# Performance work log

Hardware: AMD Instinct MI355X
Metric: run time of the kernel (lower is better)

Reference implementation:

```python
import jax, jax.numpy as jnp
import numpy as np

N, NS, D, HID = 8192, 512, 1024, 1024  # nodes, num_edges, f_dim, mlp hidden (max(f_dim,128))


def layernorm(x, g, b, eps=1e-5):
    m = x.mean(-1, keepdims=True)
    v = x.var(-1, keepdims=True)
    return (x - m) / jnp.sqrt(v + eps) * g + b


def mask_topk(a, kk):
    # keep only the top-kk entries of each row (vectorized version of mask_attn)
    _, idx = jax.lax.top_k(a, kk)
    rows = jnp.arange(a.shape[0])[:, None]
    mask = jnp.zeros(a.shape, a.dtype).at[rows, idx].set(1.0)
    return a * mask


def setup_inputs() -> dict:
    key = jax.random.key(0)
    ks = jax.random.split(key, 16)
    xavier = lambda k, i, o: jax.random.uniform(k, (i, o), jnp.float32, -1.0, 1.0) * np.sqrt(6.0 / (i + o))
    return {
        "inputs": jax.random.normal(ks[0], (N, D), jnp.float32),
        "noise": jax.random.normal(ks[1], (NS, D), jnp.float32),
        "edges_mu": jax.random.normal(ks[2], (1, D), jnp.float32),
        "edges_logsigma": xavier(ks[3], 1, D),
        "Wq": xavier(ks[4], D, D), "bq": jnp.zeros((D,), jnp.float32),
        "Wk": xavier(ks[5], D, D), "bk": jnp.zeros((D,), jnp.float32),
        "Wv": xavier(ks[6], D, D), "bv": jnp.zeros((D,), jnp.float32),
        "W1": xavier(ks[7], 2 * D, HID), "b1": jnp.zeros((HID,), jnp.float32),
        "W2": xavier(ks[8], HID, D), "b2": jnp.zeros((D,), jnp.float32),
        "g_in": jnp.ones((D,), jnp.float32), "b_in": jnp.zeros((D,), jnp.float32),
        "g_e": jnp.ones((D,), jnp.float32), "b_e": jnp.zeros((D,), jnp.float32),
        "k_n": 64,
        "k_e": 8,
    }


def reference(inputs, noise, edges_mu, edges_logsigma, Wq, bq, Wk, bk, Wv, bv,
              W1, b1, W2, b2, g_in, b_in, g_e, b_e, k_n, k_e):
    n, d = inputs.shape
    scale = d ** -0.5
    eps = 1e-8
    x = layernorm(inputs, g_in, b_in)                       # norm_input
    k = jax.nn.relu(x @ Wk + bk)                            # [N, D]
    v = jax.nn.relu(x @ Wv + bv)                            # [N, D]
    edges = edges_mu + jnp.exp(edges_logsigma) * noise      # [NS, D]
    # single iteration (iters=1)
    edges = layernorm(edges, g_e, b_e)                      # norm_edgs
    q = jax.nn.relu(edges @ Wq + bq)                        # [NS, D]
    dots = jnp.einsum('ni,mi->nm', q, k) * scale            # [NS, N]
    attn = jax.nn.softmax(dots, axis=1) + eps
    attn = attn / attn.sum(axis=1, keepdims=True)
    attn = mask_topk(attn, k_n)
    updates = jnp.einsum('nm,md->nd', attn, v)              # [NS, D]
    edges = jnp.concatenate([edges, updates], axis=1)       # [NS, 2D]
    edges = jax.nn.relu(edges @ W1 + b1) @ W2 + b2          # mlp -> [NS, D]
    q2 = x @ Wq + bq                                        # no relu in source
    k2 = jax.nn.relu(edges @ Wk + bk)                       # [NS, D]
    dots_v = jnp.einsum('ni,mi->nm', q2, k2) * scale        # [N, NS]
    attn_v = jax.nn.softmax(dots_v, axis=1)
    H = mask_topk(attn_v, k_e)
    return edges, H, dots
```

## Files before the change

### kernel.cpp

```cpp
#include <hip/hip_runtime.h>
#include <stdint.h>
#include <stddef.h>

typedef unsigned short u16;
typedef __bf16 bf16x8 __attribute__((ext_vector_type(8)));
typedef float f32x4 __attribute__((ext_vector_type(4)));

#define DEV __device__ __forceinline__

DEV float bf2f(u16 u){ union{uint32_t i; float f;} c; c.i=(uint32_t)u<<16; return c.f; }
DEV u16 f2bf(float f){ union{float f; uint32_t i;} c; c.f=f; uint32_t x=c.i;
  uint32_t r = x + 0x7FFFu + ((x>>16)&1u); return (u16)(r>>16); }
DEV uint32_t fmap(float f){ union{float f; uint32_t u;} c; c.f=f;
  return (c.u & 0x80000000u) ? ~c.u : (c.u | 0x80000000u); }
DEV float funmap(uint32_t u){ union{uint32_t u; float f;} c;
  c.u = (u & 0x80000000u) ? (u & 0x7FFFFFFFu) : ~u; return c.f; }
DEV void split2(float x, u16& h, u16& l){ h = f2bf(x); l = f2bf(x - bf2f(h)); }

DEV float bredsum(float v, float* buf, int tid){
  #pragma unroll
  for(int o=32;o;o>>=1) v += __shfl_down(v,o);
  __syncthreads();
  if((tid&63)==0) buf[tid>>6]=v;
  __syncthreads();
  return buf[0]+buf[1]+buf[2]+buf[3];
}
DEV float bredmax(float v, float* buf, int tid){
  #pragma unroll
  for(int o=32;o;o>>=1) v = fmaxf(v, __shfl_down(v,o));
  __syncthreads();
  if((tid&63)==0) buf[tid>>6]=v;
  __syncthreads();
  return fmaxf(fmaxf(buf[0],buf[1]),fmaxf(buf[2],buf[3]));
}
DEV int bredsumi(int v, int* buf, int tid){
  #pragma unroll
  for(int o=32;o;o>>=1) v += __shfl_down(v,o);
  __syncthreads();
  if((tid&63)==0) buf[tid>>6]=v;
  __syncthreads();
  return buf[0]+buf[1]+buf[2]+buf[3];
}

template<bool RELU, int SK>
__global__ __launch_bounds__(256)
void gemm1_64(const u16* __restrict__ A, int lda,
              const u16* __restrict__ Bt, int ldb,
              const float* __restrict__ bias, float scale,
              u16* __restrict__ outb, float* __restrict__ outf,
              float* __restrict__ part,
              int K, int ldc, int M)
{
  __shared__ __align__(16) u16 As[64*32];
  __shared__ __align__(16) u16 Bs[128*32];
  const int tid = threadIdx.x, lane = tid&63, wave = tid>>6;
  const int m0 = blockIdx.y*64, n0 = blockIdx.x*128;
  const int wm = (wave>>1)*32, wn = (wave&1)*64;
  const int ml = lane&15, quad = lane>>4;
  const int ks = K / SK;
  const int kbeg = blockIdx.z * ks;
  const u16* pa  = A  + (size_t)(m0+(tid>>2))*lda + kbeg + (tid&3)*8;
  const u16* pb0 = Bt + (size_t)(n0+(tid>>2))*ldb + kbeg + (tid&3)*8;
  const u16* pb1 = Bt + (size_t)(n0+64+(tid>>2))*ldb + kbeg + (tid&3)*8;

  f32x4 acc[2][4];
  #pragma unroll
  for(int i=0;i<2;i++)
    #pragma unroll
    for(int j=0;j<4;j++) acc[i][j] = (f32x4){0.f,0.f,0.f,0.f};

  uint4 ra=*(const uint4*)pa, rb0=*(const uint4*)pb0, rb1=*(const uint4*)pb1;
  for(int k0=0;k0<ks;k0+=32){
    __syncthreads();
    *(uint4*)&As[tid*8]       = ra;
    *(uint4*)&Bs[tid*8]       = rb0;
    *(uint4*)&Bs[(256+tid)*8] = rb1;
    __syncthreads();
    if(k0+32<ks){
      ra  = *(const uint4*)(pa +k0+32);
      rb0 = *(const uint4*)(pb0+k0+32);
      rb1 = *(const uint4*)(pb1+k0+32);
    }
    bf16x8 af[2], bf[4];
    #pragma unroll
    for(int mi=0;mi<2;mi++) af[mi] = *(const bf16x8*)&As[(wm+mi*16+ml)*32 + quad*8];
    #pragma unroll
    for(int ni=0;ni<4;ni++) bf[ni] = *(const bf16x8*)&Bs[(wn+ni*16+ml)*32 + quad*8];
    #pragma unroll
    for(int mi=0;mi<2;mi++)
      #pragma unroll
      for(int ni=0;ni<4;ni++)
        acc[mi][ni] = __builtin_amdgcn_mfma_f32_16x16x32_bf16(af[mi], bf[ni], acc[mi][ni], 0,0,0);
  }
  #pragma unroll
  for(int mi=0;mi<2;mi++){
    const int rbase = m0 + wm + mi*16 + quad*4;
    #pragma unroll
    for(int ni=0;ni<4;ni++){
      const int col = n0 + wn + ni*16 + ml;
      if(SK==1){
        const float bv = bias ? bias[col] : 0.f;
        #pragma unroll
        for(int r=0;r<4;r++){
          float v = acc[mi][ni][r]*scale + bv;
          if(RELU) v = fmaxf(v, 0.f);
          const size_t idx = (size_t)(rbase + r)*ldc + col;
          if(outb) outb[idx] = f2bf(v);
          if(outf) outf[idx] = v;
        }
      }else{
        #pragma unroll
        for(int r=0;r<4;r++)
          part[((size_t)blockIdx.z*M + rbase + r)*ldc + col] = acc[mi][ni][r];
      }
    }
  }
}

template<bool RELU>
__global__ __launch_bounds__(256)
void gemm1_128(const u16* __restrict__ A, int lda,
               const u16* __restrict__ Bt, int ldb,
               const float* __restrict__ bias, float scale,
               u16* __restrict__ outb, float* __restrict__ outf,
               int K, int ldc)
{
  __shared__ __align__(16) u16 As[128*32];
  __shared__ __align__(16) u16 Bs[128*32];
  const int tid = threadIdx.x, lane = tid&63, wave = tid>>6;
  const int m0 = blockIdx.y*128, n0 = blockIdx.x*128;
  const int wm = (wave>>1)*64, wn = (wave&1)*64;
  const int ml = lane&15, quad = lane>>4;
  const u16* pa0 = A  + (size_t)(m0+(tid>>2))*lda    + (tid&3)*8;
  const u16* pa1 = A  + (size_t)(m0+64+(tid>>2))*lda + (tid&3)*8;
  const u16* pb0 = Bt + (size_t)(n0+(tid>>2))*ldb    + (tid&3)*8;
  const u16* pb1 = Bt + (size_t)(n0+64+(tid>>2))*ldb + (tid&3)*8;

  f32x4 acc[4][4];
  #pragma unroll
  for(int i=0;i<4;i++)
    #pragma unroll
    for(int j=0;j<4;j++) acc[i][j] = (f32x4){0.f,0.f,0.f,0.f};

  uint4 ra0=*(const uint4*)pa0, ra1=*(const uint4*)pa1;
  uint4 rb0=*(const uint4*)pb0, rb1=*(const uint4*)pb1;
  for(int k0=0;k0<K;k0+=32){
    __syncthreads();
    *(uint4*)&As[tid*8]       = ra0;
    *(uint4*)&As[(256+tid)*8] = ra1;
    *(uint4*)&Bs[tid*8]       = rb0;
    *(uint4*)&Bs[(256+tid)*8] = rb1;
    __syncthreads();
    if(k0+32<K){
      ra0 = *(const uint4*)(pa0+k0+32);
      ra1 = *(const uint4*)(pa1+k0+32);
      rb0 = *(const uint4*)(pb0+k0+32);
      rb1 = *(const uint4*)(pb1+k0+32);
    }
    bf16x8 af[4], bf[4];
    #pragma unroll
    for(int mi=0;mi<4;mi++) af[mi] = *(const bf16x8*)&As[(wm+mi*16+ml)*32 + quad*8];
    #pragma unroll
    for(int ni=0;ni<4;ni++) bf[ni] = *(const bf16x8*)&Bs[(wn+ni*16+ml)*32 + quad*8];
    #pragma unroll
    for(int mi=0;mi<4;mi++)
      #pragma unroll
      for(int ni=0;ni<4;ni++)
        acc[mi][ni] = __builtin_amdgcn_mfma_f32_16x16x32_bf16(af[mi], bf[ni], acc[mi][ni], 0,0,0);
  }
  #pragma unroll
  for(int mi=0;mi<4;mi++){
    const int rbase = m0 + wm + mi*16 + quad*4;
    #pragma unroll
    for(int ni=0;ni<4;ni++){
      const int col = n0 + wn + ni*16 + ml;
      const float bv = bias ? bias[col] : 0.f;
      #pragma unroll
      for(int r=0;r<4;r++){
        float v = acc[mi][ni][r]*scale + bv;
        if(RELU) v = fmaxf(v, 0.f);
        const size_t idx = (size_t)(rbase + r)*ldc + col;
        if(outb) outb[idx] = f2bf(v);
        if(outf) outf[idx] = v;
      }
    }
  }
}

template<bool RELU, int SK>
__global__ __launch_bounds__(256)
void gemm3_64(const u16* __restrict__ Ah, const u16* __restrict__ Al, int lda,
              const u16* __restrict__ Bh, const u16* __restrict__ Bl, int ldb,
              const float* __restrict__ bias, float scale,
              u16* __restrict__ outh, u16* __restrict__ outl,
              float* __restrict__ outf, float* __restrict__ part,
              int K, int ldc, int M)
{
  __shared__ __align__(16) u16 AsH[64*32];
  __shared__ __align__(16) u16 AsL[64*32];
  __shared__ __align__(16) u16 BsH[128*32];
  __shared__ __align__(16) u16 BsL[128*32];
  const int tid = threadIdx.x, lane = tid&63, wave = tid>>6;
  const int m0 = blockIdx.y*64, n0 = blockIdx.x*128;
  const int wm = (wave>>1)*32, wn = (wave&1)*64;
  const int ml = lane&15, quad = lane>>4;
  const int ks = K / SK;
  const int kbeg = blockIdx.z * ks;
  const size_t ao  = (size_t)(m0+(tid>>2))*lda + kbeg + (tid&3)*8;
  const size_t bo0 = (size_t)(n0+(tid>>2))*ldb + kbeg + (tid&3)*8;
  const size_t bo1 = (size_t)(n0+64+(tid>>2))*ldb + kbeg + (tid&3)*8;

  f32x4 acc[2][4];
  #pragma unroll
  for(int i=0;i<2;i++)
    #pragma unroll
    for(int j=0;j<4;j++) acc[i][j] = (f32x4){0.f,0.f,0.f,0.f};

  uint4 rah=*(const uint4*)(Ah+ao),  ral=*(const uint4*)(Al+ao);
  uint4 rbh0=*(const uint4*)(Bh+bo0), rbl0=*(const uint4*)(Bl+bo0);
  uint4 rbh1=*(const uint4*)(Bh+bo1), rbl1=*(const uint4*)(Bl+bo1);
  for(int k0=0;k0<ks;k0+=32){
    __syncthreads();
    *(uint4*)&AsH[tid*8]       = rah;
    *(uint4*)&AsL[tid*8]       = ral;
    *(uint4*)&BsH[tid*8]       = rbh0;
    *(uint4*)&BsL[tid*8]       = rbl0;
    *(uint4*)&BsH[(256+tid)*8] = rbh1;
    *(uint4*)&BsL[(256+tid)*8] = rbl1;
    __syncthreads();
    if(k0+32<ks){
      const int s = k0+32;
      rah =*(const uint4*)(Ah+ao +s); ral =*(const uint4*)(Al+ao +s);
      rbh0=*(const uint4*)(Bh+bo0+s); rbl0=*(const uint4*)(Bl+bo0+s);
      rbh1=*(const uint4*)(Bh+bo1+s); rbl1=*(const uint4*)(Bl+bo1+s);
    }
    bf16x8 afh[2], afl[2], bfh[4], bfl[4];
    #pragma unroll
    for(int mi=0;mi<2;mi++){
      const int o = (wm+mi*16+ml)*32 + quad*8;
      afh[mi] = *(const bf16x8*)&AsH[o];
      afl[mi] = *(const bf16x8*)&AsL[o];
    }
    #pragma unroll
    for(int ni=0;ni<4;ni++){
      const int o = (wn+ni*16+ml)*32 + quad*8;
      bfh[ni] = *(const bf16x8*)&BsH[o];
      bfl[ni] = *(const bf16x8*)&BsL[o];
    }
    #pragma unroll
    for(int mi=0;mi<2;mi++)
      #pragma unroll
      for(int ni=0;ni<4;ni++){
        acc[mi][ni] = __builtin_amdgcn_mfma_f32_16x16x32_bf16(afh[mi], bfh[ni], acc[mi][ni], 0,0,0);
        acc[mi][ni] = __builtin_amdgcn_mfma_f32_16x16x32_bf16(afh[mi], bfl[ni], acc[mi][ni], 0,0,0);
        acc[mi][ni] = __builtin_amdgcn_mfma_f32_16x16x32_bf16(afl[mi], bfh[ni], acc[mi][ni], 0,0,0);
      }
  }
  #pragma unroll
  for(int mi=0;mi<2;mi++){
    const int rbase = m0 + wm + mi*16 + quad*4;
    #pragma unroll
    for(int ni=0;ni<4;ni++){
      const int col = n0 + wn + ni*16 + ml;
      if(SK==1){
        const float bv = bias ? bias[col] : 0.f;
        #pragma unroll
        for(int r=0;r<4;r++){
          float v = acc[mi][ni][r]*scale + bv;
          if(RELU) v = fmaxf(v, 0.f);
          const size_t idx = (size_t)(rbase + r)*ldc + col;
          if(outh){ u16 h, l; split2(v, h, l); outh[idx] = h; outl[idx] = l; }
          if(outf) outf[idx] = v;
        }
      }else{
        #pragma unroll
        for(int r=0;r<4;r++)
          part[((size_t)blockIdx.z*M + rbase + r)*ldc + col] = acc[mi][ni][r];
      }
    }
  }
}

__global__ __launch_bounds__(256)
void gemm3_128(const u16* __restrict__ Ah, const u16* __restrict__ Al, int lda,
               const u16* __restrict__ Bh, const u16* __restrict__ Bl, int ldb,
               const float* __restrict__ bias, float scale,
               float* __restrict__ outf, int K, int ldc)
{
  __shared__ __align__(16) u16 AsH[128*32];
  __shared__ __align__(16) u16 AsL[128*32];
  __shared__ __align__(16) u16 BsH[128*32];
  __shared__ __align__(16) u16 BsL[128*32];
  const int tid = threadIdx.x, lane = tid&63, wave = tid>>6;
  const int m0 = blockIdx.y*128, n0 = blockIdx.x*128;
  const int wm = (wave>>1)*64, wn = (wave&1)*64;
  const int ml = lane&15, quad = lane>>4;
  const size_t ao0 = (size_t)(m0+(tid>>2))*lda    + (tid&3)*8;
  const size_t ao1 = (size_t)(m0+64+(tid>>2))*lda + (tid&3)*8;
  const size_t bo0 = (size_t)(n0+(tid>>2))*ldb    + (tid&3)*8;
  const size_t bo1 = (size_t)(n0+64+(tid>>2))*ldb + (tid&3)*8;

  f32x4 acc[4][4];
  #pragma unroll
  for(int i=0;i<4;i++)
    #pragma unroll
    for(int j=0;j<4;j++) acc[i][j] = (f32x4){0.f,0.f,0.f,0.f};

  uint4 rah0=*(const uint4*)(Ah+ao0), ral0=*(const uint4*)(Al+ao0);
  uint4 rah1=*(const uint4*)(Ah+ao1), ral1=*(const uint4*)(Al+ao1);
  uint4 rbh0=*(const uint4*)(Bh+bo0), rbl0=*(const uint4*)(Bl+bo0);
  uint4 rbh1=*(const uint4*)(Bh+bo1), rbl1=*(const uint4*)(Bl+bo1);
  for(int k0=0;k0<K;k0+=32){
    __syncthreads();
    *(uint4*)&AsH[tid*8]       = rah0;
    *(uint4*)&AsH[(256+tid)*8] = rah1;
    *(uint4*)&AsL[tid*8]       = ral0;
    *(uint4*)&AsL[(256+tid)*8] = ral1;
    *(uint4*)&BsH[tid*8]       = rbh0;
    *(uint4*)&BsH[(256+tid)*8] = rbh1;
    *(uint4*)&BsL[tid*8]       = rbl0;
    *(uint4*)&BsL[(256+tid)*8] = rbl1;
    __syncthreads();
    if(k0+32<K){
      const int s = k0+32;
      rah0=*(const uint4*)(Ah+ao0+s); ral0=*(const uint4*)(Al+ao0+s);
      rah1=*(const uint4*)(Ah+ao1+s); ral1=*(const uint4*)(Al+ao1+s);
      rbh0=*(const uint4*)(Bh+bo0+s); rbl0=*(const uint4*)(Bl+bo0+s);
      rbh1=*(const uint4*)(Bh+bo1+s); rbl1=*(const uint4*)(Bl+bo1+s);
    }
    bf16x8 afh[4], afl[4], bfh[4], bfl[4];
    #pragma unroll
    for(int mi=0;mi<4;mi++){
      const int o = (wm+mi*16+ml)*32 + quad*8;
      afh[mi] = *(const bf16x8*)&AsH[o];
      afl[mi] = *(const bf16x8*)&AsL[o];
    }
    #pragma unroll
    for(int ni=0;ni<4;ni++){
      const int o = (wn+ni*16+ml)*32 + quad*8;
      bfh[ni] = *(const bf16x8*)&BsH[o];
      bfl[ni] = *(const bf16x8*)&BsL[o];
    }
    #pragma unroll
    for(int mi=0;mi<4;mi++)
      #pragma unroll
      for(int ni=0;ni<4;ni++){
        acc[mi][ni] = __builtin_amdgcn_mfma_f32_16x16x32_bf16(afh[mi], bfh[ni], acc[mi][ni], 0,0,0);
        acc[mi][ni] = __builtin_amdgcn_mfma_f32_16x16x32_bf16(afh[mi], bfl[ni], acc[mi][ni], 0,0,0);
        acc[mi][ni] = __builtin_amdgcn_mfma_f32_16x16x32_bf16(afl[mi], bfh[ni], acc[mi][ni], 0,0,0);
      }
  }
  #pragma unroll
  for(int mi=0;mi<4;mi++){
    const int rbase = m0 + wm + mi*16 + quad*4;
    #pragma unroll
    for(int ni=0;ni<4;ni++){
      const int col = n0 + wn + ni*16 + ml;
      const float bv = bias ? bias[col] : 0.f;
      #pragma unroll
      for(int r=0;r<4;r++){
        const float v = acc[mi][ni][r]*scale + bv;
        outf[(size_t)(rbase + r)*ldc + col] = v;
      }
    }
  }
}

template<bool RELU, int SK>
__global__ __launch_bounds__(256)
void reduce_epi(const float* __restrict__ part, const float* __restrict__ bias,
                float scale, u16* __restrict__ outh, u16* __restrict__ outl,
                u16* __restrict__ outb, float* __restrict__ outf,
                size_t MN, int N)
{
  const size_t i = ((size_t)blockIdx.x*256 + threadIdx.x)*4;
  float4 s = *(const float4*)(part + i);
  #pragma unroll
  for(int z=1; z<SK; z++){
    const float4 t = *(const float4*)(part + (size_t)z*MN + i);
    s.x += t.x; s.y += t.y; s.z += t.z; s.w += t.w;
  }
  const int col = (int)(i % (size_t)N);
  float4 bv = bias ? *(const float4*)(bias + col) : (float4){0.f,0.f,0.f,0.f};
  float v[4] = { s.x*scale + bv.x, s.y*scale + bv.y, s.z*scale + bv.z, s.w*scale + bv.w };
  if(RELU){
    #pragma unroll
    for(int j=0;j<4;j++) v[j] = fmaxf(v[j], 0.f);
  }
  if(outh){
    ushort4 h4, l4;
    split2(v[0], h4.x, l4.x); split2(v[1], h4.y, l4.y);
    split2(v[2], h4.z, l4.z); split2(v[3], h4.w, l4.w);
    *(ushort4*)(outh + i) = h4;
    *(ushort4*)(outl + i) = l4;
  }
  if(outb){
    ushort4 b4;
    b4.x=f2bf(v[0]); b4.y=f2bf(v[1]); b4.z=f2bf(v[2]); b4.w=f2bf(v[3]);
    *(ushort4*)(outb + i) = b4;
  }
  if(outf) *(float4*)(outf + i) = (float4){v[0],v[1],v[2],v[3]};
}

__global__ __launch_bounds__(256)
void transpose_split(const float* __restrict__ in, u16* __restrict__ outh,
                     u16* __restrict__ outl, int R, int C)
{
  __shared__ float tile[32][33];
  const int tx = threadIdx.x & 31, ty = threadIdx.x >> 5;
  const int bx = blockIdx.x*32, by = blockIdx.y*32;
  #pragma unroll
  for(int i=0;i<32;i+=8)
    tile[ty+i][tx] = in[(size_t)(by+ty+i)*C + bx + tx];
  __syncthreads();
  #pragma unroll
  for(int i=0;i<32;i+=8){
    const float v = tile[tx][ty+i];
    u16 h, l; split2(v, h, l);
    const size_t o = (size_t)(bx+ty+i)*R + by + tx;
    outh[o] = h; outl[o] = l;
  }
}
__global__ __launch_bounds__(256)
void transpose_plain(const float* __restrict__ in, u16* __restrict__ outh, int R, int C)
{
  __shared__ float tile[32][33];
  const int tx = threadIdx.x & 31, ty = threadIdx.x >> 5;
  const int bx = blockIdx.x*32, by = blockIdx.y*32;
  #pragma unroll
  for(int i=0;i<32;i+=8)
    tile[ty+i][tx] = in[(size_t)(by+ty+i)*C + bx + tx];
  __syncthreads();
  #pragma unroll
  for(int i=0;i<32;i+=8)
    outh[(size_t)(bx+ty+i)*R + by + tx] = f2bf(tile[tx][ty+i]);
}
__global__ __launch_bounds__(256)
void split_convert(const float* __restrict__ in, u16* __restrict__ oh,
                   u16* __restrict__ ol)
{
  const int i = blockIdx.x*256 + threadIdx.x;
  const float4 v = ((const float4*)in)[i];
  ushort4 h4, l4;
  split2(v.x, h4.x, l4.x); split2(v.y, h4.y, l4.y);
  split2(v.z, h4.z, l4.z); split2(v.w, h4.w, l4.w);
  ((ushort4*)oh)[i] = h4; ((ushort4*)ol)[i] = l4;
}

__global__ __launch_bounds__(256)
void layernorm_rows(const float* __restrict__ in, const float* __restrict__ g,
                    const float* __restrict__ bb, u16* __restrict__ outh,
                    u16* __restrict__ outl, int ostride)
{
  __shared__ float buf[4];
  const int row = blockIdx.x, tid = threadIdx.x;
  const float4 xv = ((const float4*)(in + (size_t)row*1024))[tid];
  float s  = bredsum(xv.x+xv.y+xv.z+xv.w, buf, tid);
  float s2 = bredsum(xv.x*xv.x+xv.y*xv.y+xv.z*xv.z+xv.w*xv.w, buf, tid);
  const float mean = s * (1.f/1024.f);
  const float var  = s2 * (1.f/1024.f) - mean*mean;
  const float rs   = 1.f / sqrtf(var + 1e-5f);
  const float4 gv = ((const float4*)g)[tid];
  const float4 bv = ((const float4*)bb)[tid];
  float o0 = (xv.x-mean)*rs*gv.x + bv.x;
  float o1 = (xv.y-mean)*rs*gv.y + bv.y;
  float o2 = (xv.z-mean)*rs*gv.z + bv.z;
  float o3 = (xv.w-mean)*rs*gv.w + bv.w;
  ushort4 oh, ol;
  split2(o0, oh.x, ol.x); split2(o1, oh.y, ol.y);
  split2(o2, oh.z, ol.z); split2(o3, oh.w, ol.w);
  ((ushort4*)(outh + (size_t)row*ostride))[tid] = oh;
  ((ushort4*)(outl + (size_t)row*ostride))[tid] = ol;
}

__global__ __launch_bounds__(256)
void edges_ln(const float* __restrict__ noise, const float* __restrict__ mu,
              const float* __restrict__ lsig, const float* __restrict__ g,
              const float* __restrict__ bb, u16* __restrict__ outh,
              u16* __restrict__ outl, int ostride)
{
  __shared__ float buf[4];
  const int row = blockIdx.x, tid = threadIdx.x;
  const float4 nv  = ((const float4*)(noise + (size_t)row*1024))[tid];
  const float4 muv = ((const float4*)mu)[tid];
  const float4 lsv = ((const float4*)lsig)[tid];
  float v0 = muv.x + expf(lsv.x)*nv.x;
  float v1 = muv.y + expf(lsv.y)*nv.y;
  float v2 = muv.z + expf(lsv.z)*nv.z;
  float v3 = muv.w + expf(lsv.w)*nv.w;
  float s  = bredsum(v0+v1+v2+v3, buf, tid);
  float s2 = bredsum(v0*v0+v1*v1+v2*v2+v3*v3, buf, tid);
  const float mean = s * (1.f/1024.f);
  const float var  = s2 * (1.f/1024.f) - mean*mean;
  const float rs   = 1.f / sqrtf(var + 1e-5f);
  const float4 gv = ((const float4*)g)[tid];
  const float4 bv = ((const float4*)bb)[tid];
  float o0 = (v0-mean)*rs*gv.x + bv.x;
  float o1 = (v1-mean)*rs*gv.y + bv.y;
  float o2 = (v2-mean)*rs*gv.z + bv.z;
  float o3 = (v3-mean)*rs*gv.w + bv.w;
  ushort4 oh, ol;
  split2(o0, oh.x, ol.x); split2(o1, oh.y, ol.y);
  split2(o2, oh.z, ol.z); split2(o3, oh.w, ol.w);
  ((ushort4*)(outh + (size_t)row*ostride))[tid] = oh;
  ((ushort4*)(outl + (size_t)row*ostride))[tid] = ol;
}

#define SWZ(i) ((i) ^ (((((unsigned)(i))>>5)&7u)<<2))
__global__ __launch_bounds__(256)
void softmax_topk_a(const float* __restrict__ dots, const int* __restrict__ knp,
                    int* __restrict__ tidx, float* __restrict__ tw)
{
  const int NC = 8192;
  __shared__ __align__(16) uint32_t us[8192];
  __shared__ float fbuf[4];
  __shared__ int ibuf[4];
  __shared__ int scan[256];
  __shared__ uint32_t hist[256];
  __shared__ uint32_t bcast;
  __shared__ int slot_ctr;
  const int row = blockIdx.x, tid = threadIdx.x;
  const int lane = tid & 63, wave = tid >> 6;
  const float* x = dots + (size_t)row * NC;

  float mx = -3.4e38f;
  #pragma unroll
  for(int it=0; it<8; ++it){
    const int i = (tid + it*256)*4;
    const float4 f = *(const float4*)(x + i);
    mx = fmaxf(fmaxf(mx, fmaxf(f.x,f.y)), fmaxf(f.z,f.w));
    uint4 u; u.x=fmap(f.x); u.y=fmap(f.y); u.z=fmap(f.z); u.w=fmap(f.w);
    *(uint4*)&us[SWZ(i)] = u;
  }
  mx = bredmax(mx, fbuf, tid);

  float se = 0.f;
  #pragma unroll
  for(int it=0; it<8; ++it){
    const int i = (tid + it*256)*4;
    const uint4 u = *(const uint4*)&us[SWZ(i)];
    se += expf(funmap(u.x)-mx) + expf(funmap(u.y)-mx)
        + expf(funmap(u.z)-mx) + expf(funmap(u.w)-mx);
  }
  se = bredsum(se, fbuf, tid);
  const float T = 1.f + (float)NC * 1e-8f;

  const int k = knp[0];
  const int base = tid*32;

  uint32_t prefix = 0;
  int remaining = k;
  #pragma unroll
  for(int shift=24; shift>=0; shift-=8){
    hist[tid] = 0;
    __syncthreads();
    const uint32_t himask = (shift==24) ? 0u : (0xFFFFFFFFu << (shift+8));
    #pragma unroll
    for(int j=0;j<32;j+=4){
      const uint4 u4 = *(const uint4*)&us[SWZ(base+j)];
      const uint32_t uu[4] = {u4.x,u4.y,u4.z,u4.w};
      #pragma unroll
      for(int t=0;t<4;t++)
        if((uu[t] & himask) == prefix) atomicAdd(&hist[(uu[t]>>shift)&255u], 1u);
    }
    __syncthreads();
    if(wave==0){
      const uint32_t h0=hist[4*lane], h1=hist[4*lane+1],
                     h2=hist[4*lane+2], h3=hist[4*lane+3];
      const uint32_t s3=h3, s2=h2+s3, s1=h1+s2, s0=h0+s1;
      uint32_t tsum = s0;
      #pragma unroll
      for(int o=1;o<64;o<<=1){
        const uint32_t vv = __shfl_down(tsum, o);
        if(lane + o < 64) tsum += vv;
      }
      const uint32_t excl = tsum - s0;
      const uint32_t r = (uint32_t)remaining;
      int cand = -1; uint32_t gsel = 0;
      if     (s3+excl >= r){ cand = 4*lane+3; gsel = excl; }
      else if(s2+excl >= r){ cand = 4*lane+2; gsel = s3+excl; }
      else if(s1+excl >= r){ cand = 4*lane+1; gsel = s2+excl; }
      else if(s0+excl >= r){ cand = 4*lane+0; gsel = s1+excl; }
      int bestc = cand; uint32_t bestg = gsel;
      #pragma unroll
      for(int o=32;o;o>>=1){
        const int oc = __shfl_xor(bestc, o);
        const uint32_t og = __shfl_xor(bestg, o);
        if(oc > bestc){ bestc = oc; bestg = og; }
      }
      if(lane==0) bcast = (uint32_t)bestc;
      remaining -= (int)bestg;
    }
    __syncthreads();
    prefix |= bcast << shift;
  }
  const uint32_t uth = prefix;

  int gt = 0, eq = 0;
  #pragma unroll
  for(int j=0;j<32;j+=4){
    const uint4 u4 = *(const uint4*)&us[SWZ(base+j)];
    gt += (u4.x>uth)+(u4.y>uth)+(u4.z>uth)+(u4.w>uth);
    eq += (u4.x==uth)+(u4.y==uth)+(u4.z==uth)+(u4.w==uth);
  }
  const int c1 = bredsumi(gt, ibuf, tid);
  __syncthreads();
  scan[tid] = eq;
  __syncthreads();
  #pragma unroll
  for(int o=1;o<256;o<<=1){
    int t = (tid>=o) ? scan[tid-o] : 0;
    __syncthreads();
    scan[tid] += t;
    __syncthreads();
  }
  int eq_rank = scan[tid] - eq;
  const int budget = k - c1;
  if(tid==0) slot_ctr = 0;
  __syncthreads();
  #pragma unroll 2
  for(int j=0;j<32;j+=4){
    const uint4 u4 = *(const uint4*)&us[SWZ(base+j)];
    const uint32_t uu[4] = {u4.x,u4.y,u4.z,u4.w};
    #pragma unroll
    for(int t=0;t<4;t++){
      const uint32_t u = uu[t];
      bool sel = (u > uth);
      if(u == uth){ sel = (eq_rank < budget); eq_rank++; }
      if(sel){
        const int s = atomicAdd(&slot_ctr, 1);
        const float f = funmap(u);
        const float w = (expf(f - mx)/se + 1e-8f) / T;
        if(s < 128){ tidx[row*128 + s] = base + j + t; tw[row*128 + s] = w; }
      }
    }
  }
}

__global__ __launch_bounds__(256)
void gather_updates(const int* __restrict__ tidx, const float* __restrict__ tw,
                    const int* __restrict__ knp, const u16* __restrict__ v,
                    u16* __restrict__ cath, u16* __restrict__ catl)
{
  __shared__ int   idx_s[128];
  __shared__ float w_s[128];
  const int row = blockIdx.x, tid = threadIdx.x;
  const int kk = knp[0];
  if(tid < 128){
    idx_s[tid] = (tid < kk) ? (tidx[row*128+tid] & 8191) : 0;
    w_s[tid]   = (tid < kk) ? tw[row*128+tid] : 0.f;
  }
  __syncthreads();
  const int c = tid*4;
  float a0=0,a1=0,a2=0,a3=0;
  for(int j=0;j<kk && j<128;j++){
    const ushort4 vv = *(const ushort4*)&v[(size_t)idx_s[j]*1024 + c];
    const float w = w_s[j];
    a0 += w*bf2f(vv.x); a1 += w*bf2f(vv.y); a2 += w*bf2f(vv.z); a3 += w*bf2f(vv.w);
  }
  ushort4 oh, ol;
  split2(a0, oh.x, ol.x); split2(a1, oh.y, ol.y);
  split2(a2, oh.z, ol.z); split2(a3, oh.w, ol.w);
  ((ushort4*)(cath + (size_t)row*2048 + 1024))[tid] = oh;
  ((ushort4*)(catl + (size_t)row*2048 + 1024))[tid] = ol;
}

__global__ __launch_bounds__(256)
void bias_v_kernel(const float* __restrict__ bq, const u16* __restrict__ k2h,
                   const u16* __restrict__ k2l, float* __restrict__ out)
{
  __shared__ float buf[4];
  const int row = blockIdx.x, tid = threadIdx.x;
  const ushort4 h4 = ((const ushort4*)(k2h + (size_t)row*1024))[tid];
  const ushort4 l4 = ((const ushort4*)(k2l + (size_t)row*1024))[tid];
  const float4 b4 = ((const float4*)bq)[tid];
  float s = b4.x*(bf2f(h4.x)+bf2f(l4.x)) + b4.y*(bf2f(h4.y)+bf2f(l4.y))
          + b4.z*(bf2f(h4.z)+bf2f(l4.z)) + b4.w*(bf2f(h4.w)+bf2f(l4.w));
  s = bredsum(s, buf, tid);
  if(tid==0) out[row] = s * 0.03125f;
}

__global__ __launch_bounds__(256)
void softmax_topk_h_wave(const float* __restrict__ dv, const int* __restrict__ kep,
                         float* __restrict__ H)
{
  const int wave = threadIdx.x >> 6, lane = threadIdx.x & 63;
  const int row = blockIdx.x*4 + wave;
  const float* x = dv + (size_t)row*512 + lane*8;
  const float4 a = *(const float4*)x;
  const float4 b = *(const float4*)(x+4);
  float vals[8] = {a.x,a.y,a.z,a.w,b.x,b.y,b.z,b.w};

  float mx = vals[0];
  #pragma unroll
  for(int j=1;j<8;j++) mx = fmaxf(mx, vals[j]);
  #pragma unroll
  for(int o=32;o;o>>=1) mx = fmaxf(mx, __shfl_xor(mx, o));
  float e[8], se = 0.f;
  #pragma unroll
  for(int j=0;j<8;j++){ e[j] = expf(vals[j]-mx); se += e[j]; }
  #pragma unroll
  for(int o=32;o;o>>=1) se += __shfl_xor(se, o);
  const float inv = 1.f/se;

  const int k = kep[0];
  unsigned int selmask = 0;
  for(int r=0;r<k;r++){
    unsigned long long best = 0;
    #pragma unroll
    for(int j=0;j<8;j++){
      if(!((selmask>>j)&1u)){
        const unsigned long long key =
          ((unsigned long long)fmap(vals[j]) << 9) | (unsigned long long)(511 - (lane*8+j));
        if(key > best) best = key;
      }
    }
    #pragma unroll
    for(int o=32;o;o>>=1){
      const unsigned long long other = __shfl_xor(best, o);
      if(other > best) best = other;
    }
    const int bidx = 511 - (int)(best & 511ull);
    if((bidx>>3) == lane) selmask |= 1u << (bidx & 7);
  }

  float4 o0, o1;
  o0.x = (selmask&  1u) ? e[0]*inv : 0.f;
  o0.y = (selmask&  2u) ? e[1]*inv : 0.f;
  o0.z = (selmask&  4u) ? e[2]*inv : 0.f;
  o0.w = (selmask&  8u) ? e[3]*inv : 0.f;
  o1.x = (selmask& 16u) ? e[4]*inv : 0.f;
  o1.y = (selmask& 32u) ? e[5]*inv : 0.f;
  o1.z = (selmask& 64u) ? e[6]*inv : 0.f;
  o1.w = (selmask&128u) ? e[7]*inv : 0.f;
  float* outp = H + (size_t)row*512 + lane*8;
  *(float4*)outp     = o0;
  *(float4*)(outp+4) = o1;
}

extern "C" void kernel_launch(void* const* d_in, const int* in_sizes, int n_in,
                              void* d_out, int out_size, void* d_ws, size_t ws_size,
                              hipStream_t stream)
{
  const float* inputs = (const float*)d_in[0];
  const float* noise  = (const float*)d_in[1];
  const float* emu    = (const float*)d_in[2];
  const float* elsig  = (const float*)d_in[3];
  const float* Wq = (const float*)d_in[4];  const float* bq = (const float*)d_in[5];
  const float* Wk = (const float*)d_in[6];  const float* bk = (const float*)d_in[7];
  const float* Wv = (const float*)d_in[8];  const float* bv = (const float*)d_in[9];
  const float* W1 = (const float*)d_in[10]; const float* b1 = (const float*)d_in[11];
  const float* W2 = (const float*)d_in[12]; const float* b2 = (const float*)d_in[13];
  const float* g_in = (const float*)d_in[14]; const float* b_in = (const float*)d_in[15];
  const float* g_e  = (const float*)d_in[16]; const float* b_e  = (const float*)d_in[17];
  const int* knp = (const int*)d_in[18];
  const int* kep = (const int*)d_in[19];

  float* out = (float*)d_out;
  float* out_edges = out;
  float* out_H     = out + 512*1024;
  float* out_dots  = out + 512*1024 + 8192*512;

  char* p = (char*)d_ws;
  const size_t MB = 1024ull*1024;
  u16* xh = (u16*)(p + 0*MB);
  u16* xl = (u16*)(p + 16*MB);
  u16* kb = (u16*)(p + 32*MB);
  u16* vb = (u16*)(p + 48*MB);
  float* dotsvf = (float*)(p + 32*MB);
  u16* WkTh = (u16*)(p + 64*MB);  u16* WkTl = (u16*)(p + 66*MB);
  u16* WvTh = (u16*)(p + 68*MB);
  u16* WqTh = (u16*)(p + 70*MB);
  u16* Wqh  = (u16*)(p + 72*MB);  u16* Wql  = (u16*)(p + 74*MB);
  u16* W1Th = (u16*)(p + 76*MB);  u16* W1Tl = (u16*)(p + 80*MB);
  u16* W2Th = (u16*)(p + 84*MB);  u16* W2Tl = (u16*)(p + 86*MB);
  u16* cath = (u16*)(p + 88*MB);  u16* catl = (u16*)(p + 90*MB);
  u16* qmb  = (u16*)(p + 92*MB);
  u16* h1h  = (u16*)(p + 93*MB);  u16* h1l  = (u16*)(p + 94*MB);
  u16* eoh  = (u16*)(p + 95*MB);  u16* eol  = (u16*)(p + 96*MB);
  u16* k2h  = (u16*)(p + 97*MB);  u16* k2l  = (u16*)(p + 98*MB);
  u16* Gth  = (u16*)(p + 99*MB);  u16* Gtl  = (u16*)(p + 100*MB);
  int*   tidx  = (int*)  (p + 101*MB);
  float* tw    = (float*)(p + 101*MB + 256*1024);
  float* biasv = (float*)(p + 101*MB + 512*1024);
  float* part  = (float*)(p + 104*MB);

  hipMemsetAsync(tidx, 0, 512ull*128*4, stream);
  hipMemsetAsync(tw,   0, 512ull*128*4, stream);

  transpose_split<<<dim3(32,32),256,0,stream>>>(Wk, WkTh, WkTl, 1024, 1024);
  transpose_split<<<dim3(32,64),256,0,stream>>>(W1, W1Th, W1Tl, 2048, 1024);
  transpose_split<<<dim3(32,32),256,0,stream>>>(W2, W2Th, W2Tl, 1024, 1024);
  transpose_plain<<<dim3(32,32),256,0,stream>>>(Wv, WvTh, 1024, 1024);
  transpose_plain<<<dim3(32,32),256,0,stream>>>(Wq, WqTh, 1024, 1024);
  split_convert<<<1024,256,0,stream>>>(Wq, Wqh, Wql);

  layernorm_rows<<<8192,256,0,stream>>>(inputs, g_in, b_in, xh, xl, 1024);
  edges_ln<<<512,256,0,stream>>>(noise, emu, elsig, g_e, b_e, cath, catl, 2048);

  const size_t MN = 512ull*1024;
  gemm1_128<true><<<dim3(8,64),256,0,stream>>>(xh,1024, WkTh,1024, bk, 1.f,
                                               kb,nullptr, 1024,1024);
  gemm1_128<true><<<dim3(8,64),256,0,stream>>>(xh,1024, WvTh,1024, bv, 1.f,
                                               vb,nullptr, 1024,1024);
  gemm1_64<false,4><<<dim3(8,8,4),256,0,stream>>>(cath,2048, WqTh,1024, nullptr, 1.f,
                                                  nullptr,nullptr, part, 1024,1024,512);
  reduce_epi<true,4><<<512,256,0,stream>>>(part, bq, 1.f, nullptr,nullptr, qmb,nullptr, MN, 1024);
  gemm1_128<false><<<dim3(64,4),256,0,stream>>>(qmb,1024, kb,1024, nullptr, 0.03125f,
                                                nullptr,out_dots, 1024,8192);
  softmax_topk_a<<<512,256,0,stream>>>(out_dots, knp, tidx, tw);
  gather_updates<<<512,256,0,stream>>>(tidx, tw, knp, vb, cath, catl);

  gemm3_64<false,4><<<dim3(8,8,4),256,0,stream>>>(cath,catl,2048, W1Th,W1Tl,2048,
                                                  nullptr,1.f, nullptr,nullptr,nullptr,
                                                  part, 2048,1024,512);
  reduce_epi<true,4><<<512,256,0,stream>>>(part, b1, 1.f, h1h,h1l, nullptr,nullptr, MN, 1024);
  gemm3_64<false,4><<<dim3(8,8,4),256,0,stream>>>(h1h,h1l,1024, W2Th,W2Tl,1024,
                                                  nullptr,1.f, nullptr,nullptr,nullptr,
                                                  part, 1024,1024,512);
  reduce_epi<false,4><<<512,256,0,stream>>>(part, b2, 1.f, eoh,eol, nullptr,out_edges, MN, 1024);
  gemm3_64<false,4><<<dim3(8,8,4),256,0,stream>>>(eoh,eol,1024, WkTh,WkTl,1024,
                                                  nullptr,1.f, nullptr,nullptr,nullptr,
                                                  part, 1024,1024,512);
  reduce_epi<true,4><<<512,256,0,stream>>>(part, bk, 1.f, k2h,k2l, nullptr,nullptr, MN, 1024);
  gemm3_64<false,4><<<dim3(8,8,4),256,0,stream>>>(k2h,k2l,1024, Wqh,Wql,1024,
                                                  nullptr,1.f, nullptr,nullptr,nullptr,
                                                  part, 1024,1024,512);
  reduce_epi<false,4><<<512,256,0,stream>>>(part, nullptr, 1.f, Gth,Gtl, nullptr,nullptr, MN, 1024);
  bias_v_kernel<<<512,256,0,stream>>>(bq, k2h, k2l, biasv);
  gemm3_128<<<dim3(4,64),256,0,stream>>>(xh,xl,1024, Gth,Gtl,1024,
                                         biasv, 0.03125f, dotsvf, 1024,512);
  softmax_topk_h_wave<<<2048,256,0,stream>>>(dotsvf, kep, out_H);
}
```

Measured before the change: 413.4 us.

## Fuse prep, layernorm, K/V GEMMs and bias-v into fewer kernel launches

```diff
diff --git a/kernel.cpp b/kernel.cpp
--- a/kernel.cpp
+++ b/kernel.cpp
@@ -187,6 +187,74 @@
   }
 }
 
+__global__ __launch_bounds__(256)
+void gemm_kv_128(const u16* __restrict__ A, int lda,
+                 const u16* __restrict__ Bt, int ldb,
+                 const float* __restrict__ bk, const float* __restrict__ bv,
+                 u16* __restrict__ kb, u16* __restrict__ vb, int K)
+{
+  __shared__ __align__(16) u16 As[128*32];
+  __shared__ __align__(16) u16 Bs[128*32];
+  const int tid = threadIdx.x, lane = tid&63, wave = tid>>6;
+  const int m0 = blockIdx.y*128, n0 = blockIdx.x*128;
+  const int wm = (wave>>1)*64, wn = (wave&1)*64;
+  const int ml = lane&15, quad = lane>>4;
+  const u16* pa0 = A  + (size_t)(m0+(tid>>2))*lda    + (tid&3)*8;
+  const u16* pa1 = A  + (size_t)(m0+64+(tid>>2))*lda + (tid&3)*8;
+  const u16* pb0 = Bt + (size_t)(n0+(tid>>2))*ldb    + (tid&3)*8;
+  const u16* pb1 = Bt + (size_t)(n0+64+(tid>>2))*ldb + (tid&3)*8;
+
+  f32x4 acc[4][4];
+  #pragma unroll
+  for(int i=0;i<4;i++)
+    #pragma unroll
+    for(int j=0;j<4;j++) acc[i][j] = (f32x4){0.f,0.f,0.f,0.f};
+
+  uint4 ra0=*(const uint4*)pa0, ra1=*(const uint4*)pa1;
+  uint4 rb0=*(const uint4*)pb0, rb1=*(const uint4*)pb1;
+  for(int k0=0;k0<K;k0+=32){
+    __syncthreads();
+    *(uint4*)&As[tid*8]       = ra0;
+    *(uint4*)&As[(256+tid)*8] = ra1;
+    *(uint4*)&Bs[tid*8]       = rb0;
+    *(uint4*)&Bs[(256+tid)*8] = rb1;
+    __syncthreads();
+    if(k0+32<K){
+      ra0 = *(const uint4*)(pa0+k0+32);
+      ra1 = *(const uint4*)(pa1+k0+32);
+      rb0 = *(const uint4*)(pb0+k0+32);
+      rb1 = *(const uint4*)(pb1+k0+32);
+    }
+    bf16x8 af[4], bf[4];
+    #pragma unroll
+    for(int mi=0;mi<4;mi++) af[mi] = *(const bf16x8*)&As[(wm+mi*16+ml)*32 + quad*8];
+    #pragma unroll
+    for(int ni=0;ni<4;ni++) bf[ni] = *(const bf16x8*)&Bs[(wn+ni*16+ml)*32 + quad*8];
+    #pragma unroll
+    for(int mi=0;mi<4;mi++)
+      #pragma unroll
+      for(int ni=0;ni<4;ni++)
+        acc[mi][ni] = __builtin_amdgcn_mfma_f32_16x16x32_bf16(af[mi], bf[ni], acc[mi][ni], 0,0,0);
+  }
+  #pragma unroll
+  for(int mi=0;mi<4;mi++){
+    const int rbase = m0 + wm + mi*16 + quad*4;
+    #pragma unroll
+    for(int ni=0;ni<4;ni++){
+      const int col = n0 + wn + ni*16 + ml;
+      const bool isv = col >= 1024;
+      const int c2 = col & 1023;
+      const float bb = isv ? bv[c2] : bk[c2];
+      u16* outp = isv ? vb : kb;
+      #pragma unroll
+      for(int r=0;r<4;r++){
+        const float v = fmaxf(acc[mi][ni][r] + bb, 0.f);
+        outp[(size_t)(rbase + r)*1024 + c2] = f2bf(v);
+      }
+    }
+  }
+}
+
 template<bool RELU, int SK>
 __global__ __launch_bounds__(256)
 void gemm3_64(const u16* __restrict__ Ah, const u16* __restrict__ Al, int lda,
@@ -371,9 +439,12 @@
 void reduce_epi(const float* __restrict__ part, const float* __restrict__ bias,
                 float scale, u16* __restrict__ outh, u16* __restrict__ outl,
                 u16* __restrict__ outb, float* __restrict__ outf,
-                size_t MN, int N)
-{
-  const size_t i = ((size_t)blockIdx.x*256 + threadIdx.x)*4;
+                size_t MN, int N,
+                const float* __restrict__ bqv, float* __restrict__ bvout)
+{
+  __shared__ float buf[4];
+  const int tid = threadIdx.x;
+  const size_t i = ((size_t)blockIdx.x*256 + tid)*4;
   float4 s = *(const float4*)(part + i);
   #pragma unroll
   for(int z=1; z<SK; z++){
@@ -400,101 +471,100 @@
     *(ushort4*)(outb + i) = b4;
   }
   if(outf) *(float4*)(outf + i) = (float4){v[0],v[1],v[2],v[3]};
-}
-
-__global__ __launch_bounds__(256)
-void transpose_split(const float* __restrict__ in, u16* __restrict__ outh,
-                     u16* __restrict__ outl, int R, int C)
-{
-  __shared__ float tile[32][33];
-  const int tx = threadIdx.x & 31, ty = threadIdx.x >> 5;
-  const int bx = blockIdx.x*32, by = blockIdx.y*32;
+  if(bvout){
+    const float4 q = *(const float4*)(bqv + col);
+    float d = q.x*v[0] + q.y*v[1] + q.z*v[2] + q.w*v[3];
+    d = bredsum(d, buf, tid);
+    if(tid==0) bvout[blockIdx.x] = d * 0.03125f;
+  }
+}
+
+DEV void dev_tsplit(const float* in, u16* oh, u16* ol, int R, int C,
+                    int bx, int by, int tid, float (*tile)[33])
+{
+  const int tx = tid & 31, ty = tid >> 5;
   #pragma unroll
   for(int i=0;i<32;i+=8)
-    tile[ty+i][tx] = in[(size_t)(by+ty+i)*C + bx + tx];
+    tile[ty+i][tx] = in[(size_t)(by*32+ty+i)*C + bx*32 + tx];
   __syncthreads();
   #pragma unroll
   for(int i=0;i<32;i+=8){
     const float v = tile[tx][ty+i];
     u16 h, l; split2(v, h, l);
-    const size_t o = (size_t)(bx+ty+i)*R + by + tx;
-    outh[o] = h; outl[o] = l;
-  }
-}
-__global__ __launch_bounds__(256)
-void transpose_plain(const float* __restrict__ in, u16* __restrict__ outh, int R, int C)
+    const size_t o = (size_t)(bx*32+ty+i)*R + by*32 + tx;
+    oh[o] = h; if(ol) ol[o] = l;
+  }
+}
+__global__ __launch_bounds__(256)
+void prep_weights(const float* __restrict__ Wk, const float* __restrict__ W1,
+                  const float* __restrict__ W2, const float* __restrict__ Wv,
+                  const float* __restrict__ Wq,
+                  u16* __restrict__ WkvTh, u16* __restrict__ WkTl,
+                  u16* __restrict__ W1Th,  u16* __restrict__ W1Tl,
+                  u16* __restrict__ W2Th,  u16* __restrict__ W2Tl,
+                  u16* __restrict__ WqTh,
+                  u16* __restrict__ Wqh,   u16* __restrict__ Wql)
 {
   __shared__ float tile[32][33];
-  const int tx = threadIdx.x & 31, ty = threadIdx.x >> 5;
-  const int bx = blockIdx.x*32, by = blockIdx.y*32;
-  #pragma unroll
-  for(int i=0;i<32;i+=8)
-    tile[ty+i][tx] = in[(size_t)(by+ty+i)*C + bx + tx];
-  __syncthreads();
-  #pragma unroll
-  for(int i=0;i<32;i+=8)
-    outh[(size_t)(bx+ty+i)*R + by + tx] = f2bf(tile[tx][ty+i]);
-}
-__global__ __launch_bounds__(256)
-void split_convert(const float* __restrict__ in, u16* __restrict__ oh,
-                   u16* __restrict__ ol)
-{
-  const int i = blockIdx.x*256 + threadIdx.x;
-  const float4 v = ((const float4*)in)[i];
-  ushort4 h4, l4;
-  split2(v.x, h4.x, l4.x); split2(v.y, h4.y, l4.y);
-  split2(v.z, h4.z, l4.z); split2(v.w, h4.w, l4.w);
-  ((ushort4*)oh)[i] = h4; ((ushort4*)ol)[i] = l4;
-}
-
-__global__ __launch_bounds__(256)
-void layernorm_rows(const float* __restrict__ in, const float* __restrict__ g,
-                    const float* __restrict__ bb, u16* __restrict__ outh,
-                    u16* __restrict__ outl, int ostride)
+  const int id = blockIdx.x, tid = threadIdx.x;
+  if(id < 1024){
+    dev_tsplit(Wk, WkvTh, WkTl, 1024, 1024, id&31, id>>5, tid, tile);
+  }else if(id < 3072){
+    const int l = id - 1024;
+    dev_tsplit(W1, W1Th, W1Tl, 2048, 1024, l&31, l>>5, tid, tile);
+  }else if(id < 4096){
+    const int l = id - 3072;
+    dev_tsplit(W2, W2Th, W2Tl, 1024, 1024, l&31, l>>5, tid, tile);
+  }else if(id < 5120){
+    const int l = id - 4096;
+    dev_tsplit(Wv, WkvTh + 1024*1024, nullptr, 1024, 1024, l&31, l>>5, tid, tile);
+  }else if(id < 6144){
+    const int l = id - 5120;
+    dev_tsplit(Wq, WqTh, nullptr, 1024, 1024, l&31, l>>5, tid, tile);
+  }else{
+    const int l = id - 6144;
+    const int i = l*256 + tid;
+    const float4 v = ((const float4*)Wq)[i];
+    ushort4 h4, l4;
+    split2(v.x, h4.x, l4.x); split2(v.y, h4.y, l4.y);
+    split2(v.z, h4.z, l4.z); split2(v.w, h4.w, l4.w);
+    ((ushort4*)Wqh)[i] = h4; ((ushort4*)Wql)[i] = l4;
+  }
+}
+
+__global__ __launch_bounds__(256)
+void ln_all(const float* __restrict__ in, const float* __restrict__ g,
+            const float* __restrict__ bb, u16* __restrict__ outh,
+            u16* __restrict__ outl,
+            const float* __restrict__ noise, const float* __restrict__ mu,
+            const float* __restrict__ lsig, const float* __restrict__ ge,
+            const float* __restrict__ be, u16* __restrict__ cath,
+            u16* __restrict__ catl)
 {
   __shared__ float buf[4];
-  const int row = blockIdx.x, tid = threadIdx.x;
-  const float4 xv = ((const float4*)(in + (size_t)row*1024))[tid];
-  float s  = bredsum(xv.x+xv.y+xv.z+xv.w, buf, tid);
-  float s2 = bredsum(xv.x*xv.x+xv.y*xv.y+xv.z*xv.z+xv.w*xv.w, buf, tid);
-  const float mean = s * (1.f/1024.f);
-  const float var  = s2 * (1.f/1024.f) - mean*mean;
-  const float rs   = 1.f / sqrtf(var + 1e-5f);
-  const float4 gv = ((const float4*)g)[tid];
-  const float4 bv = ((const float4*)bb)[tid];
-  float o0 = (xv.x-mean)*rs*gv.x + bv.x;
-  float o1 = (xv.y-mean)*rs*gv.y + bv.y;
-  float o2 = (xv.z-mean)*rs*gv.z + bv.z;
-  float o3 = (xv.w-mean)*rs*gv.w + bv.w;
-  ushort4 oh, ol;
-  split2(o0, oh.x, ol.x); split2(o1, oh.y, ol.y);
-  split2(o2, oh.z, ol.z); split2(o3, oh.w, ol.w);
-  ((ushort4*)(outh + (size_t)row*ostride))[tid] = oh;
-  ((ushort4*)(outl + (size_t)row*ostride))[tid] = ol;
-}
-
-__global__ __launch_bounds__(256)
-void edges_ln(const float* __restrict__ noise, const float* __restrict__ mu,
-              const float* __restrict__ lsig, const float* __restrict__ g,
-              const float* __restrict__ bb, u16* __restrict__ outh,
-              u16* __restrict__ outl, int ostride)
-{
-  __shared__ float buf[4];
-  const int row = blockIdx.x, tid = threadIdx.x;
-  const float4 nv  = ((const float4*)(noise + (size_t)row*1024))[tid];
-  const float4 muv = ((const float4*)mu)[tid];
-  const float4 lsv = ((const float4*)lsig)[tid];
-  float v0 = muv.x + expf(lsv.x)*nv.x;
-  float v1 = muv.y + expf(lsv.y)*nv.y;
-  float v2 = muv.z + expf(lsv.z)*nv.z;
-  float v3 = muv.w + expf(lsv.w)*nv.w;
+  const int tid = threadIdx.x;
+  const bool edge = blockIdx.x >= 8192;
+  const int row = edge ? (blockIdx.x - 8192) : blockIdx.x;
+  float v0,v1,v2,v3;
+  if(!edge){
+    const float4 xv = ((const float4*)(in + (size_t)row*1024))[tid];
+    v0=xv.x; v1=xv.y; v2=xv.z; v3=xv.w;
+  }else{
+    const float4 nv  = ((const float4*)(noise + (size_t)row*1024))[tid];
+    const float4 muv = ((const float4*)mu)[tid];
+    const float4 lsv = ((const float4*)lsig)[tid];
+    v0 = muv.x + expf(lsv.x)*nv.x;
+    v1 = muv.y + expf(lsv.y)*nv.y;
+    v2 = muv.z + expf(lsv.z)*nv.z;
+    v3 = muv.w + expf(lsv.w)*nv.w;
+  }
   float s  = bredsum(v0+v1+v2+v3, buf, tid);
   float s2 = bredsum(v0*v0+v1*v1+v2*v2+v3*v3, buf, tid);
   const float mean = s * (1.f/1024.f);
   const float var  = s2 * (1.f/1024.f) - mean*mean;
   const float rs   = 1.f / sqrtf(var + 1e-5f);
-  const float4 gv = ((const float4*)g)[tid];
-  const float4 bv = ((const float4*)bb)[tid];
+  const float4 gv = ((const float4*)(edge?ge:g))[tid];
+  const float4 bv = ((const float4*)(edge?be:bb))[tid];
   float o0 = (v0-mean)*rs*gv.x + bv.x;
   float o1 = (v1-mean)*rs*gv.y + bv.y;
   float o2 = (v2-mean)*rs*gv.z + bv.z;
@@ -502,8 +572,11 @@
   ushort4 oh, ol;
   split2(o0, oh.x, ol.x); split2(o1, oh.y, ol.y);
   split2(o2, oh.z, ol.z); split2(o3, oh.w, ol.w);
-  ((ushort4*)(outh + (size_t)row*ostride))[tid] = oh;
-  ((ushort4*)(outl + (size_t)row*ostride))[tid] = ol;
+  u16* ph = edge ? cath : outh;
+  u16* pl = edge ? catl : outl;
+  const int ostride = edge ? 2048 : 1024;
+  ((ushort4*)(ph + (size_t)row*ostride))[tid] = oh;
+  ((ushort4*)(pl + (size_t)row*ostride))[tid] = ol;
 }
 
 #define SWZ(i) ((i) ^ (((((unsigned)(i))>>5)&7u)<<2))
@@ -663,21 +736,6 @@
   split2(a2, oh.z, ol.z); split2(a3, oh.w, ol.w);
   ((ushort4*)(cath + (size_t)row*2048 + 1024))[tid] = oh;
   ((ushort4*)(catl + (size_t)row*2048 + 1024))[tid] = ol;
-}
-
-__global__ __launch_bounds__(256)
-void bias_v_kernel(const float* __restrict__ bq, const u16* __restrict__ k2h,
-                   const u16* __restrict__ k2l, float* __restrict__ out)
-{
-  __shared__ float buf[4];
-  const int row = blockIdx.x, tid = threadIdx.x;
-  const ushort4 h4 = ((const ushort4*)(k2h + (size_t)row*1024))[tid];
-  const ushort4 l4 = ((const ushort4*)(k2l + (size_t)row*1024))[tid];
-  const float4 b4 = ((const float4*)bq)[tid];
-  float s = b4.x*(bf2f(h4.x)+bf2f(l4.x)) + b4.y*(bf2f(h4.y)+bf2f(l4.y))
-          + b4.z*(bf2f(h4.z)+bf2f(l4.z)) + b4.w*(bf2f(h4.w)+bf2f(l4.w));
-  s = bredsum(s, buf, tid);
-  if(tid==0) out[row] = s * 0.03125f;
 }
 
 __global__ __launch_bounds__(256)
@@ -768,12 +826,12 @@
   u16* kb = (u16*)(p + 32*MB);
   u16* vb = (u16*)(p + 48*MB);
   float* dotsvf = (float*)(p + 32*MB);
-  u16* WkTh = (u16*)(p + 64*MB);  u16* WkTl = (u16*)(p + 66*MB);
-  u16* WvTh = (u16*)(p + 68*MB);
-  u16* WqTh = (u16*)(p + 70*MB);
-  u16* Wqh  = (u16*)(p + 72*MB);  u16* Wql  = (u16*)(p + 74*MB);
-  u16* W1Th = (u16*)(p + 76*MB);  u16* W1Tl = (u16*)(p + 80*MB);
-  u16* W2Th = (u16*)(p + 84*MB);  u16* W2Tl = (u16*)(p + 86*MB);
+  u16* WkvTh = (u16*)(p + 64*MB);
+  u16* WkTl  = (u16*)(p + 68*MB);
+  u16* WqTh  = (u16*)(p + 70*MB);
+  u16* Wqh   = (u16*)(p + 72*MB);  u16* Wql  = (u16*)(p + 74*MB);
+  u16* W1Th  = (u16*)(p + 76*MB);  u16* W1Tl = (u16*)(p + 80*MB);
+  u16* W2Th  = (u16*)(p + 84*MB);  u16* W2Tl = (u16*)(p + 86*MB);
   u16* cath = (u16*)(p + 88*MB);  u16* catl = (u16*)(p + 90*MB);
   u16* qmb  = (u16*)(p + 92*MB);
   u16* h1h  = (u16*)(p + 93*MB);  u16* h1l  = (u16*)(p + 94*MB);
@@ -785,27 +843,21 @@
   float* biasv = (float*)(p + 101*MB + 512*1024);
   float* part  = (float*)(p + 104*MB);
 
-  hipMemsetAsync(tidx, 0, 512ull*128*4, stream);
-  hipMemsetAsync(tw,   0, 512ull*128*4, stream);
-
-  transpose_split<<<dim3(32,32),256,0,stream>>>(Wk, WkTh, WkTl, 1024, 1024);
-  transpose_split<<<dim3(32,64),256,0,stream>>>(W1, W1Th, W1Tl, 2048, 1024);
-  transpose_split<<<dim3(32,32),256,0,stream>>>(W2, W2Th, W2Tl, 1024, 1024);
-  transpose_plain<<<dim3(32,32),256,0,stream>>>(Wv, WvTh, 1024, 1024);
-  transpose_plain<<<dim3(32,32),256,0,stream>>>(Wq, WqTh, 1024, 1024);
-  split_convert<<<1024,256,0,stream>>>(Wq, Wqh, Wql);
-
-  layernorm_rows<<<8192,256,0,stream>>>(inputs, g_in, b_in, xh, xl, 1024);
-  edges_ln<<<512,256,0,stream>>>(noise, emu, elsig, g_e, b_e, cath, catl, 2048);
+  hipMemsetAsync(tidx, 0, 512ull*128*4*2, stream);
+
+  prep_weights<<<7168,256,0,stream>>>(Wk, W1, W2, Wv, Wq,
+                                      WkvTh, WkTl, W1Th, W1Tl, W2Th, W2Tl,
+                                      WqTh, Wqh, Wql);
+  ln_all<<<8704,256,0,stream>>>(inputs, g_in, b_in, xh, xl,
+                                noise, emu, elsig, g_e, b_e, cath, catl);
 
   const size_t MN = 512ull*1024;
-  gemm1_128<true><<<dim3(8,64),256,0,stream>>>(xh,1024, WkTh,1024, bk, 1.f,
-                                               kb,nullptr, 1024,1024);
-  gemm1_128<true><<<dim3(8,64),256,0,stream>>>(xh,1024, WvTh,1024, bv, 1.f,
-                                               vb,nullptr, 1024,1024);
+  gemm_kv_128<<<dim3(16,64),256,0,stream>>>(xh,1024, WkvTh,1024, bk, bv,
+                                            kb, vb, 1024);
   gemm1_64<false,4><<<dim3(8,8,4),256,0,stream>>>(cath,2048, WqTh,1024, nullptr, 1.f,
                                                   nullptr,nullptr, part, 1024,1024,512);
-  reduce_epi<true,4><<<512,256,0,stream>>>(part, bq, 1.f, nullptr,nullptr, qmb,nullptr, MN, 1024);
+  reduce_epi<true,4><<<512,256,0,stream>>>(part, bq, 1.f, nullptr,nullptr, qmb,nullptr,
+                                           MN, 1024, nullptr, nullptr);
   gemm1_128<false><<<dim3(64,4),256,0,stream>>>(qmb,1024, kb,1024, nullptr, 0.03125f,
                                                 nullptr,out_dots, 1024,8192);
   softmax_topk_a<<<512,256,0,stream>>>(out_dots, knp, tidx, tw);
@@ -814,20 +866,23 @@
   gemm3_64<false,4><<<dim3(8,8,4),256,0,stream>>>(cath,catl,2048, W1Th,W1Tl,2048,
                                                   nullptr,1.f, nullptr,nullptr,nullptr,
                                                   part, 2048,1024,512);
-  reduce_epi<true,4><<<512,256,0,stream>>>(part, b1, 1.f, h1h,h1l, nullptr,nullptr, MN, 1024);
+  reduce_epi<true,4><<<512,256,0,stream>>>(part, b1, 1.f, h1h,h1l, nullptr,nullptr,
+                                           MN, 1024, nullptr, nullptr);
   gemm3_64<false,4><<<dim3(8,8,4),256,0,stream>>>(h1h,h1l,1024, W2Th,W2Tl,1024,
                                                   nullptr,1.f, nullptr,nullptr,nullptr,
                                                   part, 1024,1024,512);
-  reduce_epi<false,4><<<512,256,0,stream>>>(part, b2, 1.f, eoh,eol, nullptr,out_edges, MN, 1024);
-  gemm3_64<false,4><<<dim3(8,8,4),256,0,stream>>>(eoh,eol,1024, WkTh,WkTl,1024,
+  reduce_epi<false,4><<<512,256,0,stream>>>(part, b2, 1.f, eoh,eol, nullptr,out_edges,
+                                            MN, 1024, nullptr, nullptr);
+  gemm3_64<false,4><<<dim3(8,8,4),256,0,stream>>>(eoh,eol,1024, WkvTh,WkTl,1024,
                                                   nullptr,1.f, nullptr,nullptr,nullptr,
                                                   part, 1024,1024,512);
-  reduce_epi<true,4><<<512,256,0,stream>>>(part, bk, 1.f, k2h,k2l, nullptr,nullptr, MN, 1024);
+  reduce_epi<true,4><<<512,256,0,stream>>>(part, bk, 1.f, k2h,k2l, nullptr,nullptr,
+                                           MN, 1024, bq, biasv);
   gemm3_64<false,4><<<dim3(8,8,4),256,0,stream>>>(k2h,k2l,1024, Wqh,Wql,1024,
                                                   nullptr,1.f, nullptr,nullptr,nullptr,
                                                   part, 1024,1024,512);
-  reduce_epi<false,4><<<512,256,0,stream>>>(part, nullptr, 1.f, Gth,Gtl, nullptr,nullptr, MN, 1024);
-  bias_v_kernel<<<512,256,0,stream>>>(bq, k2h, k2l, biasv);
+  reduce_epi<false,4><<<512,256,0,stream>>>(part, nullptr, 1.f, Gth,Gtl, nullptr,nullptr,
+                                            MN, 1024, nullptr, nullptr);
   gemm3_128<<<dim3(4,64),256,0,stream>>>(xh,xl,1024, Gth,Gtl,1024,
                                          biasv, 0.03125f, dotsvf, 1024,512);
   softmax_topk_h_wave<<<2048,256,0,stream>>>(dotsvf, kep, out_H);
```

Result: faster. 389.3 us (-5.8%).
